# Optimization experiments

Measured on AMD Instinct MI355X. Metric: run time of the kernel, lower is better.

Reference implementation:

```python
import jax, jax.numpy as jnp
import numpy as np


def setup_inputs() -> dict:
    key = jax.random.key(0)
    k1, k2, k3, k4, k5 = jax.random.split(key, 5)
    B, C, V, D, O = 8, 64, 25000, 12, 64
    x = jax.random.normal(k1, (B, C, V), dtype=jnp.float32)
    nbr_idx = jax.random.randint(k2, (B, V, D), 0, V, dtype=jnp.int32)
    # true 1-ring valence in [1, D]
    deg = jax.random.randint(k3, (B, V), 1, D + 1, dtype=jnp.int32)
    # conv weight [O, C, 1, 2] flattened to [O, C, 2], fan-in init scale
    W = jax.random.normal(k4, (O, C, 2), dtype=jnp.float32) * (1.0 / np.sqrt(C * 2))
    b = jax.random.normal(k5, (O,), dtype=jnp.float32) * 0.01
    return {"x": x, "nbr_idx": nbr_idx, "deg": deg, "W": W, "b": b}


def reference(x, nbr_idx, deg, W, b):
    # x: [B, C, V]; nbr_idx: [B, V, D] padded 1-ring; deg: [B, V] valid count
    B, C, V = x.shape
    D = nbr_idx.shape[-1]
    # gather neighbor features: [B, C, V, D]
    gathered = jax.vmap(lambda xb, ib: xb[:, ib])(x, nbr_idx)
    mask = (jnp.arange(D, dtype=deg.dtype)[None, None, :] < deg[:, :, None])  # [B, V, D]
    maskf = mask.astype(x.dtype)[:, None, :, :]  # [B, 1, V, D]
    denom = jnp.maximum(deg, 1).astype(x.dtype)[:, None, :]  # [B, 1, V]
    nbr_mean = jnp.sum(gathered * maskf, axis=-1) / denom  # [B, C, V]
    # G: [B, C, V, 2] = (self feature, 1-ring mean); conv2d kernel (1,2)
    G = jnp.stack([x, nbr_mean], axis=-1)
    out = jnp.einsum('bcvk,ock->bov', G, W) + b[None, :, None]
    return out[..., None]  # [B, O, V, 1]
```

## Files before the change

### kernel.cpp

```cpp
#include <hip/hip_runtime.h>
#include <stdint.h>


#define NB 8
#define NC 64
#define NV 25000
#define ND 12
#define NO 64
#define VTILE 128
#define NGT 196
#define GVT 782

typedef uint32_t u32x4 __attribute__((ext_vector_type(4)));
typedef uint32_t u32x2 __attribute__((ext_vector_type(2)));
typedef __bf16  bf16x8 __attribute__((ext_vector_type(8)));
typedef float   f32x4  __attribute__((ext_vector_type(4)));

__device__ inline uint32_t bf16pack(float a, float b) {
    uint32_t ua = __float_as_uint(a), ub = __float_as_uint(b);
    ua = (ua + 0x7fffu + ((ua >> 16) & 1u)) >> 16;
    ub = (ub + 0x7fffu + ((ub >> 16) & 1u)) >> 16;
    return ua | (ub << 16);
}
__device__ inline float blo(uint32_t u) { return __uint_as_float(u << 16); }
__device__ inline float bhi(uint32_t u) { return __uint_as_float(u & 0xffff0000u); }

__global__ __launch_bounds__(256) void wt_kernel(const float* __restrict__ W,
                                                 uint32_t* __restrict__ Wcb) {
    int i = blockIdx.x * 256 + threadIdx.x;
    int m = i >> 5;
    int c = (i & 31) * 2;
    int k = m >> 6;
    int o = m & 63;
    float s0 = W[o * (NC * 2) + c * 2 + k];
    float s1 = W[o * (NC * 2) + (c + 1) * 2 + k];
    Wcb[i] = bf16pack(s0, s1);
}

__global__ __launch_bounds__(256) void ygemm_mfma(const float* __restrict__ x,
                                                  const uint32_t* __restrict__ Wcb,
                                                  const float* __restrict__ bias,
                                                  uint32_t* __restrict__ y0,
                                                  uint32_t* __restrict__ y1) {
    __shared__ uint32_t xt[VTILE * 36];

    const int b = blockIdx.x & 7;
    const int tile = blockIdx.x >> 3;
    const int vbase = tile * VTILE;
    const int tid = threadIdx.x;
    const int lane = tid & 63, wave = tid >> 6;
    const float* xb = x + (size_t)b * NC * NV;

    uint32_t* xw = xt + wave * (32 * 36);

    {
        const int vl = lane & 31;
        const int ph = lane >> 5;
        int vg = vbase + wave * 32 + vl;
        if (vg >= NV) vg = NV - 1;
#pragma unroll
        for (int r = 0; r < 16; ++r) {
            const int p = r * 2 + ph;
            const int c = p * 2;
            float s0 = __builtin_nontemporal_load(xb + (size_t)c * NV + vg);
            float s1 = __builtin_nontemporal_load(xb + (size_t)(c + 1) * NV + vg);
            xw[vl * 36 + p] = bf16pack(s0, s1);
        }
    }

    const int l15 = lane & 15, lq = lane >> 4;

    union BF { u32x4 q; bf16x8 v; } bf[2][2];
#pragma unroll
    for (int s = 0; s < 2; ++s) {
        const int rloc = s * 16 + l15;
#pragma unroll
        for (int kt = 0; kt < 2; ++kt)
            bf[s][kt].q = *reinterpret_cast<const u32x4*>(&xw[rloc * 36 + kt * 16 + lq * 4]);
    }

    f32x4 acc[2][8];
#pragma unroll
    for (int s = 0; s < 2; ++s)
#pragma unroll
        for (int mt = 0; mt < 8; ++mt) acc[s][mt] = (f32x4){0.f, 0.f, 0.f, 0.f};

#pragma unroll
    for (int kt = 0; kt < 2; ++kt) {
#pragma unroll
        for (int mt = 0; mt < 8; ++mt) {
            union { u32x4 q; bf16x8 v; } au;
            au.q = *(const u32x4*)(Wcb + (size_t)(mt * 16 + l15) * 32 + kt * 16 + lq * 4);
#pragma unroll
            for (int s = 0; s < 2; ++s)
                acc[s][mt] = __builtin_amdgcn_mfma_f32_16x16x32_bf16(au.v, bf[s][kt].v,
                                                                     acc[s][mt], 0, 0, 0);
        }
    }

#pragma unroll
    for (int s = 0; s < 2; ++s) {
        const int v = vbase + wave * 32 + s * 16 + l15;
        if (v < NV) {
            uint32_t* yr0 = y0 + ((size_t)b * NV + v) * 32;
            uint32_t* yr1 = y1 + ((size_t)b * NV + v) * 32;
#pragma unroll
            for (int mt = 0; mt < 8; ++mt) {
                const int mo = mt * 16 + lq * 4;
                f32x4 a = acc[s][mt];
                if (mt < 4) {
                    const float* bp = bias + mo;
                    a[0] += bp[0]; a[1] += bp[1]; a[2] += bp[2]; a[3] += bp[3];
                    u32x2 p = {bf16pack(a[0], a[1]), bf16pack(a[2], a[3])};
                    __builtin_nontemporal_store(p, (u32x2*)(yr0 + (mo >> 1)));
                } else {
                    u32x2 p = {bf16pack(a[0], a[1]), bf16pack(a[2], a[3])};
                    *(u32x2*)(yr1 + ((mo - 64) >> 1)) = p;
                }
            }
        }
    }
}

__global__ __launch_bounds__(256) void gather_out(const int* __restrict__ nbr,
                                                  const int* __restrict__ deg,
                                                  const uint32_t* __restrict__ y0,
                                                  const uint32_t* __restrict__ y1,
                                                  float* __restrict__ out) {
    __shared__ float lds[32 * 68];

    const int b = blockIdx.x & 7;
    const int tile = blockIdx.x >> 3;
    const int lane = threadIdx.x & 63;
    const int wave = threadIdx.x >> 6;
    const int s = lane >> 3;
    const int j = lane & 7;
    const int vloc = wave * 8 + s;
    const int v = tile * 32 + vloc;
    const int vc = v < NV ? v : NV - 1;
    const size_t bv = (size_t)b * NV + vc;

    int idxr[ND];
    {
        const int4* p = reinterpret_cast<const int4*>(nbr + bv * ND);
        int4 a0 = p[0], a1 = p[1], a2 = p[2];
        idxr[0] = a0.x; idxr[1] = a0.y; idxr[2]  = a0.z; idxr[3]  = a0.w;
        idxr[4] = a1.x; idxr[5] = a1.y; idxr[6]  = a1.z; idxr[7]  = a1.w;
        idxr[8] = a2.x; idxr[9] = a2.y; idxr[10] = a2.z; idxr[11] = a2.w;
    }
    const int dg = deg[bv];
    const float inv = 1.0f / (float)dg;
    const uint32_t* y1b = y1 + (size_t)b * NV * 32;

    u32x4 su = __builtin_nontemporal_load(
        reinterpret_cast<const u32x4*>(y0 + bv * 32) + j);

    u32x4 rows[ND];
#pragma unroll
    for (int d = 0; d < ND; ++d) {
        if (d < dg)
            rows[d] = *(reinterpret_cast<const u32x4*>(y1b + (size_t)idxr[d] * 32) + j);
    }

    float ns[8];
#pragma unroll
    for (int t = 0; t < 8; ++t) ns[t] = 0.0f;
#pragma unroll
    for (int d = 0; d < ND; ++d) {
        if (d < dg) {
            u32x4 u = rows[d];
            ns[0] += blo(u[0]); ns[1] += bhi(u[0]);
            ns[2] += blo(u[1]); ns[3] += bhi(u[1]);
            ns[4] += blo(u[2]); ns[5] += bhi(u[2]);
            ns[6] += blo(u[3]); ns[7] += bhi(u[3]);
        }
    }

    {
        float f[8];
        f[0] = __builtin_fmaf(inv, ns[0], blo(su[0]));
        f[1] = __builtin_fmaf(inv, ns[1], bhi(su[0]));
        f[2] = __builtin_fmaf(inv, ns[2], blo(su[1]));
        f[3] = __builtin_fmaf(inv, ns[3], bhi(su[1]));
        f[4] = __builtin_fmaf(inv, ns[4], blo(su[2]));
        f[5] = __builtin_fmaf(inv, ns[5], bhi(su[2]));
        f[6] = __builtin_fmaf(inv, ns[6], blo(su[3]));
        f[7] = __builtin_fmaf(inv, ns[7], bhi(su[3]));
        f32x4 w0 = {f[0], f[1], f[2], f[3]};
        f32x4 w1 = {f[4], f[5], f[6], f[7]};
        *reinterpret_cast<f32x4*>(&lds[vloc * 68 + j * 8])     = w0;
        *reinterpret_cast<f32x4*>(&lds[vloc * 68 + j * 8 + 4]) = w1;
    }
    __syncthreads();

    {
        const int vl = threadIdx.x & 31;
        const int o8 = threadIdx.x >> 5;
        const int vv = tile * 32 + vl;
        if (vv < NV) {
            float* ob = out + (size_t)b * NO * NV + vv;
#pragma unroll
            for (int oo = 0; oo < 8; ++oo) {
                const int o = oo * 8 + o8;
                __builtin_nontemporal_store(lds[vl * 68 + o], ob + (size_t)o * NV);
            }
        }
    }
}

__global__ __launch_bounds__(64) void fallback_kernel(const float* __restrict__ x,
                                                      const int* __restrict__ nbr,
                                                      const int* __restrict__ deg,
                                                      const float* __restrict__ W,
                                                      const float* __restrict__ bias,
                                                      float* __restrict__ out) {
    const int bvi = blockIdx.x;
    const int b = bvi / NV, v = bvi % NV;
    const int o = threadIdx.x;
    const int degv = deg[bvi];
    const float inv = 1.0f / (float)degv;
    float acc = bias[o];
    for (int c = 0; c < NC; ++c) {
        const float* xc = x + ((size_t)b * NC + c) * NV;
        float m = 0.0f;
        for (int d = 0; d < degv; ++d) m += xc[nbr[(size_t)bvi * ND + d]];
        acc += W[o * (NC * 2) + c * 2] * xc[v] + W[o * (NC * 2) + c * 2 + 1] * (m * inv);
    }
    out[((size_t)b * NO + o) * NV + v] = acc;
}

extern "C" void kernel_launch(void* const* d_in, const int* in_sizes, int n_in,
                              void* d_out, int out_size, void* d_ws, size_t ws_size,
                              hipStream_t stream) {
    const float* x    = (const float*)d_in[0];
    const int*   nbr  = (const int*)d_in[1];
    const int*   deg  = (const int*)d_in[2];
    const float* W    = (const float*)d_in[3];
    const float* bias = (const float*)d_in[4];
    float* out = (float*)d_out;

    const size_t wcb_dw = 4096;
    const size_t yplane = (size_t)NB * NV * 32;
    const size_t need = (wcb_dw + 2 * yplane) * 4;
    if (ws_size >= need) {
        uint32_t* Wcb = (uint32_t*)d_ws;
        uint32_t* y0 = Wcb + wcb_dw;
        uint32_t* y1 = y0 + yplane;
        wt_kernel<<<dim3(16), 256, 0, stream>>>(W, Wcb);
        ygemm_mfma<<<dim3(NB * NGT), 256, 0, stream>>>(x, Wcb, bias, y0, y1);
        gather_out<<<dim3(NB * GVT), 256, 0, stream>>>(nbr, deg, y0, y1, out);
    } else {
        fallback_kernel<<<dim3(NB * NV), 64, 0, stream>>>(x, nbr, deg, W, bias, out);
    }
}
```

Before: 171.4 us.

## Split x transpose to bf16 into separate kernel before MFMA GEMM

Adds an xt_kernel that transposes x from channel-major fp32 to vertex-major packed bf16 rows through LDS, then a new ygemm2 that loads its MFMA B operands directly from global without LDS staging. The aim is to make the GEMM kernel lighter and give it higher occupancy, and to make the transpose coalesced on both sides. The cost is an extra kernel launch plus a 6.4 MB bf16 intermediate written and read back. This path needs more workspace and falls back to the old path when that is unavailable.

Measured after the change: 174.8 us. About the same (+2.0%).

```diff
diff --git a/kernel.cpp b/kernel.cpp
--- a/kernel.cpp
+++ b/kernel.cpp
@@ -8,7 +8,9 @@
 #define ND 12
 #define NO 64
 #define VTILE 128
+#define VROW 32
 #define NGT 196
+#define XTT 391
 #define GVT 782
 
 typedef uint32_t u32x4 __attribute__((ext_vector_type(4)));
@@ -37,6 +39,107 @@
     Wcb[i] = bf16pack(s0, s1);
 }
 
+__global__ __launch_bounds__(256) void xt_kernel(const float* __restrict__ x,
+                                                 uint32_t* __restrict__ xt) {
+    __shared__ float lds[64 * 65];
+    const int b = blockIdx.x & 7;
+    const int tile = blockIdx.x >> 3;
+    const int vbase = tile * 64;
+    const int t = threadIdx.x;
+    const int lane = t & 63, wave = t >> 6;
+    const float* xb = x + (size_t)b * NC * NV;
+
+    int vg = vbase + lane;
+    if (vg >= NV) vg = NV - 1;
+#pragma unroll
+    for (int r = 0; r < 16; ++r) {
+        const int c = wave * 16 + r;
+        lds[c * 65 + lane] = __builtin_nontemporal_load(xb + (size_t)c * NV + vg);
+    }
+    __syncthreads();
+
+    const int vl = t >> 2;
+    const int q  = t & 3;
+    const int vo = vbase + vl;
+    if (vo < NV) {
+        uint32_t w[8];
+#pragma unroll
+        for (int i = 0; i < 8; ++i) {
+            const int c = q * 16 + i * 2;
+            w[i] = bf16pack(lds[c * 65 + vl], lds[(c + 1) * 65 + vl]);
+        }
+        uint32_t* dst = xt + ((size_t)b * NV + vo) * VROW + q * 8;
+        *reinterpret_cast<u32x4*>(dst)     = (u32x4){w[0], w[1], w[2], w[3]};
+        *reinterpret_cast<u32x4*>(dst + 4) = (u32x4){w[4], w[5], w[6], w[7]};
+    }
+}
+
+__global__ __launch_bounds__(256, 4) void ygemm2(const uint32_t* __restrict__ xt,
+                                                 const uint32_t* __restrict__ Wcb,
+                                                 const float* __restrict__ bias,
+                                                 uint32_t* __restrict__ y0,
+                                                 uint32_t* __restrict__ y1) {
+    const int b = blockIdx.x & 7;
+    const int tile = blockIdx.x >> 3;
+    const int vbase = tile * VTILE;
+    const int lane = threadIdx.x & 63, wave = threadIdx.x >> 6;
+    const int l15 = lane & 15, lq = lane >> 4;
+    const uint32_t* xtb = xt + (size_t)b * NV * VROW;
+
+    union BF { u32x4 q; bf16x8 v; } bf[2][2];
+#pragma unroll
+    for (int s = 0; s < 2; ++s) {
+        int v = vbase + wave * 32 + s * 16 + l15;
+        if (v >= NV) v = NV - 1;
+        const uint32_t* xr = xtb + (size_t)v * VROW;
+#pragma unroll
+        for (int kt = 0; kt < 2; ++kt)
+            bf[s][kt].q = *reinterpret_cast<const u32x4*>(xr + kt * 16 + lq * 4);
+    }
+
+    f32x4 acc[2][8];
+#pragma unroll
+    for (int s = 0; s < 2; ++s)
+#pragma unroll
+        for (int mt = 0; mt < 8; ++mt) acc[s][mt] = (f32x4){0.f, 0.f, 0.f, 0.f};
+
+#pragma unroll
+    for (int kt = 0; kt < 2; ++kt) {
+#pragma unroll
+        for (int mt = 0; mt < 8; ++mt) {
+            union { u32x4 q; bf16x8 v; } au;
+            au.q = *(const u32x4*)(Wcb + (size_t)(mt * 16 + l15) * 32 + kt * 16 + lq * 4);
+#pragma unroll
+            for (int s = 0; s < 2; ++s)
+                acc[s][mt] = __builtin_amdgcn_mfma_f32_16x16x32_bf16(au.v, bf[s][kt].v,
+                                                                     acc[s][mt], 0, 0, 0);
+        }
+    }
+
+#pragma unroll
+    for (int s = 0; s < 2; ++s) {
+        const int v = vbase + wave * 32 + s * 16 + l15;
+        if (v < NV) {
+            uint32_t* yr0 = y0 + ((size_t)b * NV + v) * 32;
+            uint32_t* yr1 = y1 + ((size_t)b * NV + v) * 32;
+#pragma unroll
+            for (int mt = 0; mt < 8; ++mt) {
+                const int mo = mt * 16 + lq * 4;
+                f32x4 a = acc[s][mt];
+                if (mt < 4) {
+                    const float* bp = bias + mo;
+                    a[0] += bp[0]; a[1] += bp[1]; a[2] += bp[2]; a[3] += bp[3];
+                    u32x2 p = {bf16pack(a[0], a[1]), bf16pack(a[2], a[3])};
+                    __builtin_nontemporal_store(p, (u32x2*)(yr0 + (mo >> 1)));
+                } else {
+                    u32x2 p = {bf16pack(a[0], a[1]), bf16pack(a[2], a[3])};
+                    *(u32x2*)(yr1 + ((mo - 64) >> 1)) = p;
+                }
+            }
+        }
+    }
+}
+
 __global__ __launch_bounds__(256) void ygemm_mfma(const float* __restrict__ x,
                                                   const uint32_t* __restrict__ Wcb,
                                                   const float* __restrict__ bias,
@@ -52,7 +155,6 @@
     const float* xb = x + (size_t)b * NC * NV;
 
     uint32_t* xw = xt + wave * (32 * 36);
-
     {
         const int vl = lane & 31;
         const int ph = lane >> 5;
@@ -69,7 +171,6 @@
     }
 
     const int l15 = lane & 15, lq = lane >> 4;
-
     union BF { u32x4 q; bf16x8 v; } bf[2][2];
 #pragma unroll
     for (int s = 0; s < 2; ++s) {
@@ -241,8 +342,18 @@
 
     const size_t wcb_dw = 4096;
     const size_t yplane = (size_t)NB * NV * 32;
-    const size_t need = (wcb_dw + 2 * yplane) * 4;
-    if (ws_size >= need) {
+    const size_t need_full = (wcb_dw + 3 * yplane) * 4;
+    const size_t need_mid  = (wcb_dw + 2 * yplane) * 4;
+    if (ws_size >= need_full) {
+        uint32_t* Wcb = (uint32_t*)d_ws;
+        uint32_t* xtb = Wcb + wcb_dw;
+        uint32_t* y0  = xtb + yplane;
+        uint32_t* y1  = y0 + yplane;
+        wt_kernel<<<dim3(16), 256, 0, stream>>>(W, Wcb);
+        xt_kernel<<<dim3(NB * XTT), 256, 0, stream>>>(x, xtb);
+        ygemm2<<<dim3(NB * NGT), 256, 0, stream>>>(xtb, Wcb, bias, y0, y1);
+        gather_out<<<dim3(NB * GVT), 256, 0, stream>>>(nbr, deg, y0, y1, out);
+    } else if (ws_size >= need_mid) {
         uint32_t* Wcb = (uint32_t*)d_ws;
         uint32_t* y0 = Wcb + wcb_dw;
         uint32_t* y1 = y0 + yplane;
```
